# Performance work log

Hardware: AMD Instinct MI355X
Metric: run time of the kernel (lower is better)

## Reference

```python
import jax, jax.numpy as jnp
import numpy as np

N, A, AD, D, H, KTOP = 5, 900, 8, 256, 8, 300


def _bbox_min_max(anchor):
    # anchor: [N,A,8] = x,y,z,logw,logl,logh,sin_yaw,cos_yaw
    xyz = anchor[..., :3]
    w, l, h = [jnp.exp(anchor[..., i]) for i in (3, 4, 5)]
    sy, cy = anchor[..., 6], anchor[..., 7]
    yaw = jnp.arctan2(sy, cy)
    ca, sa = jnp.abs(jnp.cos(yaw)), jnp.abs(jnp.sin(yaw))
    ex = 0.5 * (l * ca + w * sa)
    ey = 0.5 * (l * sa + w * ca)
    half = jnp.stack([ex, ey, 0.5 * h], axis=-1)
    return xyz - half, xyz + half


def _forward(i2j_anchor, b_anchor, b_feature, transform_matrix, anchor_embed,
             w_roi, b_roi, bn_g, bn_b, fc1_w, fc1_b, fc2_w, fc2_b,
             anc_w, anc_b, lam_w, lam_b, wq, bq, wk, bk, wv, bv, wo, bo,
             ln_g, ln_b, K):
    n, a, ad = b_anchor.shape
    d = b_feature.shape[-1]
    heads = lam_w.shape[-1]
    dh = d // heads
    # ROI scoring + topk selection of anchors to broadcast to neighbors
    roi = jax.nn.sigmoid(b_feature @ w_roi + b_roi)[..., 0]              # [N,A]
    top_scores, top_idx = jax.lax.top_k(roi, K)                          # [N,K]
    conf = top_scores > 0.5                                              # [N,K]
    nbr = jnp.take_along_axis(b_feature, top_idx[..., None], axis=1)     # [N,K,D]
    idx4 = jnp.broadcast_to(top_idx[None, :, :, None], (n, n, K, ad))
    i2j_sel = jnp.take_along_axis(i2j_anchor, idx4, axis=2)              # [N,N,K,AD]
    # remove self (eye-mask): off-diagonal j per row i, row-major order
    offdiag = np.array([[j for j in range(n) if j != i] for i in range(n)])
    rows = np.arange(n)[:, None]
    m = K * (n - 1)
    i2j_rm = i2j_sel[rows, offdiag].reshape(n, m, ad)                    # [N,M,AD]
    tm_rm = transform_matrix[rows, offdiag]                              # [N,N-1,4,4]
    key_feat = nbr[offdiag].reshape(n, m, d)                             # [N,M,D]
    conf_rm = conf[offdiag].reshape(n, m, 1)
    nf_masked = key_feat * conf_rm
    # bbox-range masked aggregation of neighbor features into ego anchors
    mn, mx = _bbox_min_max(b_anchor)                                     # [N,A,3]
    centers = i2j_rm[..., :3]                                            # [N,M,3]
    inside = jnp.all((centers[:, None, :, :] >= mn[:, :, None, :]) &
                     (centers[:, None, :, :] <= mx[:, :, None, :]), axis=-1)  # [N,A,M]
    agg = jnp.einsum('nam,nmd->nad', inside.astype(b_feature.dtype), nf_masked)
    is_greater_than_range = ~jnp.any(inside, axis=1)                     # [N,M]
    b_feature = b_feature + agg
    # transform-matrix encoding: first 3 rows of 4x4 -> BN -> MLP
    mlp_in = tm_rm[:, :, :3, :].reshape(-1, 12)
    mu = mlp_in.mean(0)
    var = mlp_in.var(0)
    xbn = (mlp_in - mu) / jnp.sqrt(var + 1e-5) * bn_g + bn_b
    t = jax.nn.relu(xbn @ fc1_w + fc1_b) @ fc2_w + fc2_b                 # [N*(N-1),D]
    trans_enc = jnp.repeat(t.reshape(n, n - 1, 1, d), K, axis=2).reshape(n, m, d)
    key_pos = i2j_rm @ anc_w + anc_b + trans_enc                         # anchorencoder + trans
    # distance-biased attention mask
    diff = b_anchor[:, :, None, :2] - i2j_rm[:, None, :, :2]
    dist = jnp.sqrt(jnp.sum(diff * diff, axis=-1) + 1e-12)               # cdist [N,A,M]
    lm = (b_feature @ lam_w + lam_b).transpose(0, 2, 1)                  # [N,H,A]
    bias = -jnp.log1p(dist)[:, None, :, :] * lm[..., None]               # [N,H,A,M]
    # multi-head attention (query=b_feature(+anchor_embed pos), key/value=neighbors)
    q = b_feature + anchor_embed
    k = key_feat + key_pos
    v = key_feat
    qh = (q @ wq + bq).reshape(n, a, heads, dh)
    kh = (k @ wk + bk).reshape(n, m, heads, dh)
    vh = (v @ wv + bv).reshape(n, m, heads, dh)
    logits = jnp.einsum('nahd,nmhd->nham', qh, kh) / np.sqrt(dh).astype(np.float32) + bias
    attn = jax.nn.softmax(logits, axis=-1)
    out = jnp.einsum('nham,nmhd->nahd', attn, vh).reshape(n, a, d) @ wo + bo
    res = b_feature + out                                                # residual (identity=query)
    mu2 = res.mean(-1, keepdims=True)
    var2 = res.var(-1, keepdims=True)
    return (res - mu2) / jnp.sqrt(var2 + 1e-5) * ln_g + ln_b


def setup_inputs() -> dict:
    key = jax.random.key(0)
    ks = jax.random.split(key, 24)
    s = 0.05
    inp = {
        'i2j_anchor': jax.random.normal(ks[0], (N, N, A, AD), jnp.float32),
        'b_anchor': jax.random.normal(ks[1], (N, A, AD), jnp.float32),
        'b_feature': jax.random.normal(ks[2], (N, A, D), jnp.float32),
        'transform_matrix': jax.random.normal(ks[3], (N, N, 4, 4), jnp.float32),
        'anchor_embed': jax.random.normal(ks[4], (N, A, D), jnp.float32),
        'w_roi': jax.random.normal(ks[5], (D, 1), jnp.float32) * s,
        'b_roi': jnp.zeros((1,), jnp.float32),
        'bn_g': jnp.ones((12,), jnp.float32),
        'bn_b': jnp.zeros((12,), jnp.float32),
        'fc1_w': jax.random.normal(ks[6], (12, D), jnp.float32) * s,
        'fc1_b': jnp.zeros((D,), jnp.float32),
        'fc2_w': jax.random.normal(ks[7], (D, D), jnp.float32) * s,
        'fc2_b': jnp.zeros((D,), jnp.float32),
        'anc_w': jax.random.normal(ks[8], (AD, D), jnp.float32) * s,
        'anc_b': jnp.zeros((D,), jnp.float32),
        'lam_w': jax.random.normal(ks[9], (D, H), jnp.float32) * s,
        'lam_b': jnp.zeros((H,), jnp.float32),
        'wq': jax.random.normal(ks[10], (D, D), jnp.float32) * s,
        'bq': jnp.zeros((D,), jnp.float32),
        'wk': jax.random.normal(ks[11], (D, D), jnp.float32) * s,
        'bk': jnp.zeros((D,), jnp.float32),
        'wv': jax.random.normal(ks[12], (D, D), jnp.float32) * s,
        'bv': jnp.zeros((D,), jnp.float32),
        'wo': jax.random.normal(ks[13], (D, D), jnp.float32) * s,
        'bo': jnp.zeros((D,), jnp.float32),
        'ln_g': jnp.ones((D,), jnp.float32),
        'ln_b': jnp.zeros((D,), jnp.float32),
        'K': KTOP,
    }
    return inp


def reference(i2j_anchor, b_anchor, b_feature, transform_matrix, anchor_embed,
              w_roi, b_roi, bn_g, bn_b, fc1_w, fc1_b, fc2_w, fc2_b,
              anc_w, anc_b, lam_w, lam_b, wq, bq, wk, bk, wv, bv, wo, bo,
              ln_g, ln_b, K):
    return _forward(i2j_anchor, b_anchor, b_feature, transform_matrix, anchor_embed,
                    w_roi, b_roi, bn_g, bn_b, fc1_w, fc1_b, fc2_w, fc2_b,
                    anc_w, anc_b, lam_w, lam_b, wq, bq, wk, bk, wv, bv, wo, bo,
                    ln_g, ln_b, K)
```

## Files before the change

### kernel.cpp

```cpp
#include <hip/hip_runtime.h>
#include <math.h>

#define N_ 5
#define A_ 900
#define AD_ 8
#define D_ 256
#define H_ 8
#define DH_ 32
#define K_ 300
#define NM1_ 4
#define M_ 1200
#define MP_ 1216
#define KC_ 64
#define HALF_ 600
#define NCHUNK2_ 10
#define SCOREB_ 1125

typedef _Float16 f16x8 __attribute__((ext_vector_type(8)));
typedef _Float16 f16x4 __attribute__((ext_vector_type(4)));
typedef float f32x4 __attribute__((ext_vector_type(4)));

#define LOG2E_ 1.4426950408889634f

__global__ __launch_bounds__(256) void scoremlp_kernel(const float* __restrict__ bf,
                                                       const float* __restrict__ w,
                                                       const float* __restrict__ b,
                                                       const float* __restrict__ tm,
                                                       const float* __restrict__ bn_g, const float* __restrict__ bn_b,
                                                       const float* __restrict__ fc1_w, const float* __restrict__ fc1_b,
                                                       const float* __restrict__ fc2_w, const float* __restrict__ fc2_b,
                                                       float* __restrict__ scores,
                                                       float* __restrict__ t_out) {
  int bid = blockIdx.x;
  int t = threadIdx.x;
  if (bid < SCOREB_) {
    int wid = t >> 6, lane = t & 63;
    int row = bid * 4 + wid;
    if (row >= N_ * A_) return;
    const float* x = bf + (long)row * D_;
    float dot = 0.f;
#pragma unroll
    for (int e = 0; e < 4; e++) dot += x[lane + 64 * e] * w[lane + 64 * e];
#pragma unroll
    for (int o = 32; o; o >>= 1) dot += __shfl_xor(dot, o, 64);
    if (lane == 0) scores[row] = dot + b[0];
  } else {
    int r = bid - SCOREB_;
    __shared__ float x2[20][12];
    __shared__ float y2[12];
    __shared__ float hbuf[D_];
    if (t < 240) {
      int rr = t / 12, f = t % 12;
      int i = rr / NM1_, jj = rr % NM1_;
      int j = jj < i ? jj : jj + 1;
      x2[rr][f] = tm[((long)(i * N_ + j) * 4 + (f / 4)) * 4 + (f % 4)];
    }
    __syncthreads();
    if (t < 12) {
      float s = 0.f;
      for (int rr = 0; rr < 20; rr++) s += x2[rr][t];
      float m = s / 20.0f;
      float v = 0.f;
      for (int rr = 0; rr < 20; rr++) { float d = x2[rr][t] - m; v += d * d; }
      v /= 20.0f;
      y2[t] = (x2[r][t] - m) * rsqrtf(v + 1e-5f) * bn_g[t] + bn_b[t];
    }
    __syncthreads();
    float acc = fc1_b[t];
#pragma unroll
    for (int f = 0; f < 12; f++) acc += y2[f] * fc1_w[f * D_ + t];
    hbuf[t] = fmaxf(acc, 0.0f);
    __syncthreads();
    float acc2 = fc2_b[t];
    for (int k = 0; k < D_; k++) acc2 += hbuf[k] * fc2_w[k * D_ + t];
    t_out[r * D_ + t] = acc2;
  }
}

__global__ __launch_bounds__(1024) void topk_kernel(const float* __restrict__ scores,
                                                    int* __restrict__ top_idx,
                                                    float* __restrict__ conf) {
  __shared__ float sc[1024];
  __shared__ int si[1024];
  int i = blockIdx.x, t = threadIdx.x;
  sc[t] = (t < A_) ? scores[i * A_ + t] : -INFINITY;
  si[t] = t;
  __syncthreads();
  for (int k = 2; k <= 1024; k <<= 1) {
    for (int j = k >> 1; j > 0; j >>= 1) {
      int ixj = t ^ j;
      if (ixj > t) {
        bool dir = ((t & k) == 0);
        float a = sc[t], b = sc[ixj];
        bool sw = dir ? (a < b) : (a > b);
        if (sw) {
          sc[t] = b; sc[ixj] = a;
          int tmp = si[t]; si[t] = si[ixj]; si[ixj] = tmp;
        }
      }
      __syncthreads();
    }
  }
  if (t < K_) {
    top_idx[i * K_ + t] = si[t];
    conf[i * K_ + t] = sc[t] > 0.0f ? 1.0f : 0.0f;
  }
}

#define GKT_ 10
__global__ __launch_bounds__(256) void gather_kernel(const float* __restrict__ b_feature,
                                                     const float* __restrict__ i2j_anchor,
                                                     const int* __restrict__ top_idx,
                                                     const float* __restrict__ conf,
                                                     const float* __restrict__ anc_w,
                                                     const float* __restrict__ anc_b,
                                                     const float* __restrict__ t_mlp,
                                                     _Float16* __restrict__ key_feat16,
                                                     float* __restrict__ conf_rm,
                                                     float* __restrict__ i2j_rm,
                                                     _Float16* __restrict__ key_in16) {
  int blk = blockIdx.x;
  int i = blk / NM1_, jj = blk % NM1_;
  int j = jj < i ? jj : jj + 1;
  int k0 = blockIdx.y * GKT_;
  int c = threadIdx.x;
  __shared__ float aw[AD_][D_];
#pragma unroll
  for (int r = 0; r < AD_; r++) aw[r][c] = anc_w[r * D_ + c];
  float ab = anc_b[c];
  float tv = t_mlp[(i * NM1_ + jj) * D_ + c];
  __syncthreads();
  for (int k = k0; k < k0 + GKT_; k++) {
    int idx = top_idx[j * K_ + k];
    float cf = conf[j * K_ + k];
    const float* src = b_feature + ((long)(j * A_ + idx)) * D_;
    float val = src[c];
    long mrow = (long)i * M_ + jj * K_ + k;
    key_feat16[mrow * D_ + c] = (_Float16)val;
    const float* ap = i2j_anchor + ((long)((i * N_ + j) * A_ + idx)) * AD_;
    if (c < AD_) i2j_rm[mrow * AD_ + c] = ap[c];
    if (c == 0) conf_rm[mrow] = cf;
    float pos = ab + tv;
#pragma unroll
    for (int r = 0; r < AD_; r++) pos += ap[r] * aw[r][c];
    key_in16[mrow * D_ + c] = (_Float16)(val + pos);
  }
}

__global__ __launch_bounds__(256) void trans_kernel(const float* __restrict__ w0, const float* __restrict__ w1,
                                                    const float* __restrict__ w2, const float* __restrict__ w3,
                                                    const _Float16* __restrict__ kf,
                                                    _Float16* __restrict__ wT, _Float16* __restrict__ kT) {
  int bid = blockIdx.x;
  int t = threadIdx.x;
  if (bid < 64) {
    int y = bid >> 4, tile = bid & 15;
    const float* src = (y == 0) ? w0 : (y == 1) ? w1 : (y == 2) ? w2 : w3;
    _Float16* dst = wT + (size_t)y * D_ * D_;
    int kr = (tile >> 2) * 64, nc = (tile & 3) * 64;
    __shared__ float lds[64][65];
#pragma unroll
    for (int r = 0; r < 16; r++) {
      int row = r * 4 + (t >> 6), col = t & 63;
      lds[row][col] = src[(size_t)(kr + row) * D_ + nc + col];
    }
    __syncthreads();
#pragma unroll
    for (int r = 0; r < 16; r++) {
      int orow = r * 4 + (t >> 6), ocol = t & 63;
      dst[(size_t)(nc + orow) * D_ + kr + ocol] = (_Float16)lds[ocol][orow];
    }
  } else {
    int b = bid - 64;
    int i = b / 76, rem = b % 76;
    int m0 = (rem % 19) * 64, d0 = (rem / 19) * 64;
    __shared__ _Float16 lds2[64][66];
    const _Float16* src = kf + (size_t)i * M_ * D_;
    _Float16* dst = kT + (size_t)i * D_ * M_;
#pragma unroll
    for (int r = 0; r < 16; r++) {
      int row = r * 4 + (t >> 6), col = t & 63;
      int m = m0 + row;
      lds2[row][col] = (m < M_) ? src[(size_t)m * D_ + d0 + col] : (_Float16)0.0f;
    }
    __syncthreads();
#pragma unroll
    for (int r = 0; r < 16; r++) {
      int orow = r * 4 + (t >> 6), ocol = t & 63;
      int m = m0 + ocol;
      if (m < M_) dst[(size_t)(d0 + orow) * M_ + m] = lds2[ocol][orow];
    }
  }
}

__global__ __launch_bounds__(256) void insbias_kernel(const float* __restrict__ i2j_rm,
                                                      const float* __restrict__ conf_rm,
                                                      const float* __restrict__ ban,
                                                      _Float16* __restrict__ inside,
                                                      _Float16* __restrict__ Lbuf) {
  int i = blockIdx.x;
  int g = blockIdx.y;
  __shared__ float cx[M_], cy[M_], cz[M_], cf[M_];
  for (int m = threadIdx.x; m < M_; m += 256) {
    const float* cp = i2j_rm + ((long)i * M_ + m) * AD_;
    cx[m] = cp[0]; cy[m] = cp[1]; cz[m] = cp[2];
    cf[m] = conf_rm[(long)i * M_ + m];
  }
  __syncthreads();
#pragma unroll
  for (int r = 0; r < 4; r++) {
    int a = g * 4 + r;
    int row = i * A_ + a;
    const float* ap = ban + (long)row * AD_;
    float ax = ap[0], ay = ap[1], az = ap[2];
    float w = expf(ap[3]), l = expf(ap[4]), hh = expf(ap[5]);
    float yaw = atan2f(ap[6], ap[7]);
    float ca = fabsf(cosf(yaw)), sa = fabsf(sinf(yaw));
    float ex = 0.5f * (l * ca + w * sa);
    float ey = 0.5f * (l * sa + w * ca);
    float ez = 0.5f * hh;
    float mn0 = ax - ex, mn1 = ay - ey, mn2 = az - ez;
    float mx0 = ax + ex, mx1 = ay + ey, mx2 = az + ez;
    _Float16* ldst = Lbuf + (size_t)row * MP_;
    _Float16* idst = inside + (size_t)row * M_;
    for (int m = threadIdx.x; m < M_; m += 256) {
      float c0 = cx[m], c1 = cy[m], c2 = cz[m];
      bool ins = (c0 >= mn0) && (c0 <= mx0) && (c1 >= mn1) && (c1 <= mx1) && (c2 >= mn2) && (c2 <= mx2);
      idst[m] = ins ? (_Float16)cf[m] : (_Float16)0.0f;
      float dx = ax - c0, dy = ay - c1;
      ldst[m] = (_Float16)log1pf(sqrtf(dx * dx + dy * dy + 1e-12f));
    }
  }
}

#define GLD_ 74
template <typename TO, bool HAS_BIAS, bool HAS_RES, bool VTRANS = false>
__device__ __forceinline__ void gemm_tile_body(
    const _Float16* __restrict__ A, int lda, int Mr,
    const _Float16* __restrict__ B, int ldb,
    const float* __restrict__ bias, const float* __restrict__ res,
    TO* __restrict__ C, int ldc,
    int m0, int n0, int k_begin, int k_end) {
  __shared__ _Float16 As[64 * GLD_];
  __shared__ _Float16 Bs[64 * GLD_];
  int tid = threadIdx.x;
  int lane = tid & 63;
  int wid = tid >> 6;
  int wr = (wid >> 1) * 32, wc = (wid & 1) * 32;
  int lr = lane & 15, lk = (lane >> 4) * 8;
  int srow = tid >> 3;
  int scol = (tid & 7) * 8;
  f16x8 aR[2], bR[2];
  f16x8 zero8 = {};
  auto loadg = [&](int kb) {
#pragma unroll
    for (int r = 0; r < 2; r++) {
      int gm = m0 + srow + r * 32;
      int gk = kb + scol;
      aR[r] = (gm < Mr && gk < k_end) ? *(const f16x8*)&A[(size_t)gm * lda + gk] : zero8;
      int gn = n0 + srow + r * 32;
      bR[r] = (gk < k_end) ? *(const f16x8*)&B[(size_t)gn * ldb + gk] : zero8;
    }
  };
  auto store_lds = [&]() {
#pragma unroll
    for (int r = 0; r < 2; r++) {
      *(f16x8*)&As[(srow + r * 32) * GLD_ + scol] = aR[r];
      *(f16x8*)&Bs[(srow + r * 32) * GLD_ + scol] = bR[r];
    }
  };
  f32x4 acc[2][2] = {};
  int niter = (k_end - k_begin + 63) >> 6;
  loadg(k_begin);
  store_lds();
  __syncthreads();
  for (int it = 0; it < niter; ++it) {
    bool more = (it + 1 < niter);
    if (more) loadg(k_begin + (it + 1) * 64);
#pragma unroll
    for (int ks = 0; ks < 2; ks++) {
      f16x8 af[2], bf[2];
#pragma unroll
      for (int mi = 0; mi < 2; mi++) af[mi] = *(const f16x8*)&As[(wr + mi * 16 + lr) * GLD_ + ks * 32 + lk];
#pragma unroll
      for (int ni = 0; ni < 2; ni++) bf[ni] = *(const f16x8*)&Bs[(wc + ni * 16 + lr) * GLD_ + ks * 32 + lk];
#pragma unroll
      for (int mi = 0; mi < 2; mi++)
#pragma unroll
        for (int ni = 0; ni < 2; ni++)
          acc[mi][ni] = __builtin_amdgcn_mfma_f32_16x16x32_f16(af[mi], bf[ni], acc[mi][ni], 0, 0, 0);
    }
    __syncthreads();
    if (more) { store_lds(); __syncthreads(); }
  }
  if (VTRANS) {
#pragma unroll
    for (int mi = 0; mi < 2; mi++)
#pragma unroll
      for (int ni = 0; ni < 2; ni++)
#pragma unroll
        for (int rr = 0; rr < 4; rr++) {
          int ml = wr + mi * 16 + (lane >> 4) * 4 + rr;
          int dl = wc + ni * 16 + lr;
          float v = acc[mi][ni][rr];
          if (HAS_BIAS) v += bias[n0 + dl];
          As[dl * 72 + ml] = (_Float16)v;
        }
    __syncthreads();
    int dl = tid >> 2, mp = (tid & 3) * 16;
    int gd = n0 + dl;
#pragma unroll
    for (int e8 = 0; e8 < 2; e8++) {
      int gm = m0 + mp + e8 * 8;
      if (gm < Mr) {
        int ii = gm / M_, mm = gm - ii * M_;
        *(f16x8*)&((_Float16*)C)[(size_t)(ii * D_ + gd) * ldc + mm] =
            *(const f16x8*)&As[dl * 72 + mp + e8 * 8];
      }
    }
    return;
  }
#pragma unroll
  for (int mi = 0; mi < 2; mi++)
#pragma unroll
    for (int ni = 0; ni < 2; ni++)
#pragma unroll
      for (int rr = 0; rr < 4; rr++) {
        int row = m0 + wr + mi * 16 + (lane >> 4) * 4 + rr;
        int col = n0 + wc + ni * 16 + lr;
        if (row < Mr) {
          float v = acc[mi][ni][rr];
          if (HAS_BIAS) v += bias[col];
          if (HAS_RES) v += res[(size_t)row * ldc + col];
          C[(size_t)row * ldc + col] = (TO)v;
        }
      }
}

__global__ __launch_bounds__(256) void agg_kernel(const _Float16* __restrict__ inside16,
                                                  const _Float16* __restrict__ kT16,
                                                  float* __restrict__ partial) {
  int i = blockIdx.z >> 2, sk = blockIdx.z & 3;
  int kb = sk * 320;
  int ke = kb + 320 < M_ ? kb + 320 : M_;
  gemm_tile_body<float, false, false>(
      inside16 + (size_t)i * A_ * M_, M_, A_,
      kT16 + (size_t)i * D_ * M_, M_,
      nullptr, nullptr,
      partial + (size_t)(sk * N_ + i) * A_ * D_, D_,
      blockIdx.x * 64, blockIdx.y * 64, kb, ke);
}

__global__ __launch_bounds__(256) void agg_reduce(const float* __restrict__ partial,
                                                  const float* __restrict__ b_feature,
                                                  const float* __restrict__ anchor_embed,
                                                  const float* __restrict__ lam_w,
                                                  const float* __restrict__ lam_b,
                                                  float* __restrict__ bf_upd,
                                                  _Float16* __restrict__ qin16,
                                                  float* __restrict__ lm_rm) {
  int wid = threadIdx.x >> 6, lane = threadIdx.x & 63;
  int rg = blockIdx.x * 4 + wid;
  int d0 = lane * 4;
  float lw[4][8];
#pragma unroll
  for (int e = 0; e < 4; e++) {
#pragma unroll
    for (int h = 0; h < 8; h++) lw[e][h] = lam_w[(d0 + e) * 8 + h];
  }
  float4 s = *(const float4*)&partial[(size_t)rg * D_ + d0];
#pragma unroll
  for (int sk = 1; sk < 4; sk++) {
    float4 p = *(const float4*)&partial[((size_t)sk * N_ * A_ + rg) * D_ + d0];
    s.x += p.x; s.y += p.y; s.z += p.z; s.w += p.w;
  }
  float4 bf = *(const float4*)&b_feature[(size_t)rg * D_ + d0];
  s.x += bf.x; s.y += bf.y; s.z += bf.z; s.w += bf.w;
  *(float4*)&bf_upd[(size_t)rg * D_ + d0] = s;
  float4 ae = *(const float4*)&anchor_embed[(size_t)rg * D_ + d0];
  f16x4 q4;
  q4[0] = (_Float16)(s.x + ae.x); q4[1] = (_Float16)(s.y + ae.y);
  q4[2] = (_Float16)(s.z + ae.z); q4[3] = (_Float16)(s.w + ae.w);
  *(f16x4*)&qin16[(size_t)rg * D_ + d0] = q4;
  float sv[4] = {s.x, s.y, s.z, s.w};
  float acc[8] = {};
#pragma unroll
  for (int e = 0; e < 4; e++)
#pragma unroll
    for (int h = 0; h < 8; h++) acc[h] += sv[e] * lw[e][h];
#pragma unroll
  for (int h = 0; h < 8; h++) {
#pragma unroll
    for (int o = 32; o; o >>= 1) acc[h] += __shfl_xor(acc[h], o, 64);
  }
  if (lane == 0) {
#pragma unroll
    for (int h = 0; h < 8; h++) lm_rm[(size_t)rg * H_ + h] = acc[h] + lam_b[h];
  }
}

__global__ __launch_bounds__(256) void qkv_kernel(const _Float16* __restrict__ qA,
                                                  const _Float16* __restrict__ kA,
                                                  const _Float16* __restrict__ vA,
                                                  const _Float16* __restrict__ wT,
                                                  const float* __restrict__ bq,
                                                  const float* __restrict__ bk,
                                                  const float* __restrict__ bv,
                                                  _Float16* __restrict__ qC,
                                                  _Float16* __restrict__ kC,
                                                  _Float16* __restrict__ vT) {
  int bid = blockIdx.x;
  if (bid < 284) {
    int mt = bid % 71, nt = bid / 71;
    gemm_tile_body<_Float16, true, false>(qA, D_, 4500, wT, D_, bq, nullptr, qC, D_,
                                          mt * 64, nt * 64, 0, D_);
  } else if (bid < 660) {
    int t = bid - 284;
    int mt = t % 94, nt = t / 94;
    gemm_tile_body<_Float16, true, false>(kA, D_, 6000, wT + D_ * D_, D_, bk, nullptr, kC, D_,
                                          mt * 64, nt * 64, 0, D_);
  } else {
    int t = bid - 660;
    int mt = t % 94, nt = t / 94;
    gemm_tile_body<_Float16, true, false, true>(vA, D_, 6000, wT + 2 * D_ * D_, D_, bv, nullptr, vT, MP_,
                                                mt * 64, nt * 64, 0, D_);
  }
}

__global__ __launch_bounds__(256) void outp_kernel(const _Float16* __restrict__ att16,
                                                   const _Float16* __restrict__ woT,
                                                   float* __restrict__ partial2) {
  int bid = blockIdx.x;
  int sk = bid >= 284 ? 1 : 0;
  int t = bid - sk * 284;
  int mt = t % 71, nt = t / 71;
  gemm_tile_body<float, false, false>(att16, D_, 4500, woT, D_, nullptr, nullptr,
                                      partial2 + (size_t)sk * 4500 * D_, D_,
                                      mt * 64, nt * 64, sk * 128, sk * 128 + 128);
}

#define LQP_ 72
#define LKS_ 40
#define THR2_ 11.5f
__global__ __launch_bounds__(256) void attn_mfma(const _Float16* __restrict__ qh16,
                                                 const _Float16* __restrict__ kh16,
                                                 const _Float16* __restrict__ vhT,
                                                 const float* __restrict__ lm_rm,
                                                 const _Float16* __restrict__ Lbuf,
                                                 float* __restrict__ part_ms,
                                                 float* __restrict__ part_o) {
  int bid = blockIdx.x;
  int wgid = (bid & 7) * 150 + (bid >> 3);
  int ih = wgid / 30;
  int rest = wgid % 30;
  int half = rest / 15, qt = rest % 15;
  int i = ih >> 3, h = ih & 7;
  int a0 = qt * 64;
  int mbase = half * HALF_;
  int mlimit = mbase + HALF_;

  __shared__ _Float16 QP[64 * LQP_];
  __shared__ _Float16 Ks[2][64 * LKS_];
  __shared__ _Float16 Vs[2][32 * LQP_];
  __shared__ float lmvs[64];

  int tid = threadIdx.x;
  int lane = tid & 63;
  int w16 = (tid >> 6) * 16;
  int lr = lane & 15;
  int lk = (lane >> 4) * 8;
  int mq = (lane >> 4) * 4;
  int srow = tid >> 2, spiece = tid & 3;
  int vrow = tid >> 3, vpc = (tid & 7) * 8;

  {
    int aq = a0 + srow;
    int a_ld = aq < A_ ? aq : A_ - 1;
    const uint4* src = (const uint4*)(qh16 + ((long)(i * A_ + a_ld) * D_ + h * DH_));
    *(uint4*)&QP[srow * LQP_ + spiece * 8] = src[spiece];
  }
  if (tid < 64) {
    int aq = a0 + tid;
    int a_ld = aq < A_ ? aq : A_ - 1;
    lmvs[tid] = lm_rm[(long)(i * A_ + a_ld) * H_ + h];
  }

  int qrow = w16 + lr;
  const _Float16* kb = kh16 + (long)i * M_ * D_ + h * DH_;
  const _Float16* vb = vhT + (size_t)(i * D_ + h * DH_) * MP_;
  const _Float16* lq;
  {
    int aq = a0 + qrow;
    int a_ld = aq < A_ ? aq : A_ - 1;
    lq = Lbuf + (size_t)(i * A_ + a_ld) * MP_ + mq;
  }

  uint4 kvR;
  f16x8 vvR;
  f16x4 lR[4];
  auto loadr = [&](int c) {
    int m0 = mbase + c * KC_;
    int mrow = m0 + srow;
    kvR = (mrow < M_) ? ((const uint4*)(kb + (long)mrow * D_))[spiece] : make_uint4(0, 0, 0, 0);
    vvR = *(const f16x8*)&vb[(size_t)vrow * MP_ + m0 + vpc];
#pragma unroll
    for (int mb = 0; mb < 4; mb++) lR[mb] = *(const f16x4*)&lq[m0 + mb * 16];
  };

  __syncthreads();

  float lmv2 = lmvs[qrow] * LOG2E_;
  f16x8 qa = *(const f16x8*)&QP[qrow * LQP_ + lk];

  float m_run = -INFINITY, s_part = 0.0f;
  f32x4 oacc[2] = {};

  loadr(0);

  const float SC2 = 0.17677669529663687f * LOG2E_;

  auto chunk_body = [&](int c, bool masked) {
    int m0 = mbase + c * KC_;
    int cur = c & 1;
    *(uint4*)&Ks[cur][srow * LKS_ + spiece * 8] = kvR;
    *(f16x8*)&Vs[cur][vrow * LQP_ + vpc] = vvR;
    f16x4 lcur[4];
#pragma unroll
    for (int mb = 0; mb < 4; mb++) lcur[mb] = lR[mb];
    if (c + 1 < NCHUNK2_) loadr(c + 1);
    __syncthreads();

    f32x4 sacc[4];
#pragma unroll
    for (int mb = 0; mb < 4; mb++) {
      f16x8 kf = *(const f16x8*)&Ks[cur][(mb * 16 + lr) * LKS_ + lk];
      sacc[mb] = __builtin_amdgcn_mfma_f32_16x16x32_f16(kf, qa, (f32x4){0.f, 0.f, 0.f, 0.f}, 0, 0, 0);
    }

    float lg[4][4];
#pragma unroll
    for (int mb = 0; mb < 4; mb++) {
#pragma unroll
      for (int rr = 0; rr < 4; rr++) {
        float v = sacc[mb][rr] * SC2 - (float)lcur[mb][rr] * lmv2;
        if (masked) {
          int mcol = m0 + mb * 16 + mq + rr;
          v = (mcol < mlimit) ? v : -INFINITY;
        }
        lg[mb][rr] = v;
      }
    }
    float cm = -INFINITY;
#pragma unroll
    for (int mb = 0; mb < 4; mb++)
#pragma unroll
      for (int rr = 0; rr < 4; rr++) cm = fmaxf(cm, lg[mb][rr]);
    cm = fmaxf(cm, __shfl_xor(cm, 16, 64));
    cm = fmaxf(cm, __shfl_xor(cm, 32, 64));

    bool upd = !__all(cm - m_run <= THR2_);
    float corr = 1.0f;
    if (upd) {
      float nm = fmaxf(m_run, cm);
      corr = exp2f(m_run - nm);
      m_run = nm;
      lmvs[qrow] = corr;
    }
    float ps = 0.0f;
#pragma unroll
    for (int mb = 0; mb < 4; mb++) {
      f16x4 p4;
#pragma unroll
      for (int rr = 0; rr < 4; rr++) {
        float p = exp2f(lg[mb][rr] - m_run);
        ps += p;
        p4[rr] = (_Float16)p;
      }
      *(f16x4*)&QP[qrow * LQP_ + mb * 16 + mq] = p4;
    }
    if (upd) {
      float4 c4 = *(const float4*)&lmvs[w16 + mq];
      s_part = s_part * corr + ps;
      oacc[0][0] *= c4.x; oacc[0][1] *= c4.y; oacc[0][2] *= c4.z; oacc[0][3] *= c4.w;
      oacc[1][0] *= c4.x; oacc[1][1] *= c4.y; oacc[1][2] *= c4.z; oacc[1][3] *= c4.w;
    } else {
      s_part += ps;
    }

#pragma unroll
    for (int ks = 0; ks < 2; ks++) {
      f16x8 pa = *(const f16x8*)&QP[(w16 + lr) * LQP_ + ks * 32 + lk];
#pragma unroll
      for (int db = 0; db < 2; db++) {
        f16x8 vf = *(const f16x8*)&Vs[cur][(db * 16 + lr) * LQP_ + ks * 32 + lk];
        oacc[db] = __builtin_amdgcn_mfma_f32_16x16x32_f16(pa, vf, oacc[db], 0, 0, 0);
      }
    }
  };

  for (int c = 0; c < NCHUNK2_ - 1; c++) chunk_body(c, false);
  chunk_body(NCHUNK2_ - 1, true);

  float st = s_part;
  st += __shfl_xor(st, 16, 64);
  st += __shfl_xor(st, 32, 64);

  size_t base = (size_t)(half * 40 + ih) * A_;
  if (lane < 16) {
    int a = a0 + w16 + lane;
    if (a < A_) {
      part_ms[(base + a) * 2 + 0] = m_run;
      part_ms[(base + a) * 2 + 1] = st;
    }
  }
#pragma unroll
  for (int r = 0; r < 4; r++) {
    int a = a0 + w16 + mq + r;
    if (a < A_) {
      size_t rowb = base + a;
      part_o[rowb * 32 + lr] = oacc[0][r];
      part_o[rowb * 32 + 16 + lr] = oacc[1][r];
    }
  }
}

__global__ __launch_bounds__(256) void attn_merge(const float* __restrict__ part_ms,
                                                  const float* __restrict__ part_o,
                                                  _Float16* __restrict__ att16) {
  int t = threadIdx.x;
  int R = blockIdx.x * 8 + (t >> 5);
  int d = t & 31;
  int ih = R / A_, a = R % A_;
  int i = ih >> 3, h = ih & 7;
  size_t r0 = (size_t)ih * A_ + a;
  size_t r1 = (size_t)(40 + ih) * A_ + a;
  float m0 = part_ms[r0 * 2], s0 = part_ms[r0 * 2 + 1];
  float m1 = part_ms[r1 * 2], s1 = part_ms[r1 * 2 + 1];
  float M = fmaxf(m0, m1);
  float e0 = exp2f(m0 - M), e1 = exp2f(m1 - M);
  float inv = 1.0f / (s0 * e0 + s1 * e1);
  float o = part_o[r0 * 32 + d] * e0 + part_o[r1 * 32 + d] * e1;
  att16[((size_t)(i * A_ + a)) * D_ + h * DH_ + d] = (_Float16)(o * inv);
}

__global__ __launch_bounds__(256) void ln_kernel(const float* __restrict__ partial2,
                                                 const float* __restrict__ bo,
                                                 const float* __restrict__ resid,
                                                 const float* __restrict__ g,
                                                 const float* __restrict__ b,
                                                 float* __restrict__ out) {
  int row = blockIdx.x;
  int t = threadIdx.x;
  size_t idx = (size_t)row * D_ + t;
  float v = partial2[idx] + partial2[(size_t)4500 * D_ + idx] + bo[t] + resid[idx];
  float s = v, sq = v * v;
#pragma unroll
  for (int o = 32; o; o >>= 1) {
    s += __shfl_xor(s, o, 64);
    sq += __shfl_xor(sq, o, 64);
  }
  __shared__ float ss[4], ssq[4];
  int wid = t >> 6, lane = t & 63;
  if (lane == 0) { ss[wid] = s; ssq[wid] = sq; }
  __syncthreads();
  float ts = ss[0] + ss[1] + ss[2] + ss[3];
  float tq = ssq[0] + ssq[1] + ssq[2] + ssq[3];
  float mean = ts / (float)D_;
  float var = tq / (float)D_ - mean * mean;
  out[idx] = (v - mean) * rsqrtf(var + 1e-5f) * g[t] + b[t];
}

extern "C" void kernel_launch(void* const* d_in, const int* in_sizes, int n_in,
                              void* d_out, int out_size, void* d_ws, size_t ws_size,
                              hipStream_t stream) {
  const float* i2j_anchor   = (const float*)d_in[0];
  const float* b_anchor     = (const float*)d_in[1];
  const float* b_feature    = (const float*)d_in[2];
  const float* tm           = (const float*)d_in[3];
  const float* anchor_embed = (const float*)d_in[4];
  const float* w_roi  = (const float*)d_in[5];
  const float* b_roi  = (const float*)d_in[6];
  const float* bn_g   = (const float*)d_in[7];
  const float* bn_b   = (const float*)d_in[8];
  const float* fc1_w  = (const float*)d_in[9];
  const float* fc1_b  = (const float*)d_in[10];
  const float* fc2_w  = (const float*)d_in[11];
  const float* fc2_b  = (const float*)d_in[12];
  const float* anc_w  = (const float*)d_in[13];
  const float* anc_b  = (const float*)d_in[14];
  const float* lam_w  = (const float*)d_in[15];
  const float* lam_b  = (const float*)d_in[16];
  const float* wq = (const float*)d_in[17];
  const float* bq = (const float*)d_in[18];
  const float* wk = (const float*)d_in[19];
  const float* bk = (const float*)d_in[20];
  const float* wv = (const float*)d_in[21];
  const float* bv = (const float*)d_in[22];
  const float* wo = (const float*)d_in[23];
  const float* bo = (const float*)d_in[24];
  const float* ln_g = (const float*)d_in[25];
  const float* ln_b = (const float*)d_in[26];

  float* ws = (float*)d_ws;
  size_t off = 0;
  auto alloc = [&](size_t n) { float* p = ws + off; off += (n + 3) & ~(size_t)3; return p; };

  float* scores     = alloc(N_ * A_);
  int*   top_idx    = (int*)alloc(N_ * K_);
  float* conf       = alloc(N_ * K_);
  float* t_mlp      = alloc(20 * D_);
  float* conf_rm    = alloc((size_t)N_ * M_);
  float* i2j_rm     = alloc((size_t)N_ * M_ * AD_);
  _Float16* key_feat16 = (_Float16*)alloc((size_t)N_ * M_ * D_ / 2);
  _Float16* key_in16   = (_Float16*)alloc((size_t)N_ * M_ * D_ / 2);
  _Float16* kT16       = (_Float16*)alloc((size_t)N_ * D_ * M_ / 2);
  _Float16* inside16   = (_Float16*)alloc((size_t)N_ * A_ * M_ / 2);
  _Float16* wT16       = (_Float16*)alloc((size_t)4 * D_ * D_ / 2);
  _Float16* Lbuf16     = (_Float16*)alloc((size_t)N_ * A_ * MP_ / 2 + 16);
  float* partial    = alloc((size_t)4 * N_ * A_ * D_);
  float* bf_upd     = alloc((size_t)N_ * A_ * D_);
  _Float16* qin16   = (_Float16*)alloc((size_t)N_ * A_ * D_ / 2);
  _Float16* qh16    = (_Float16*)alloc((size_t)N_ * A_ * D_ / 2);
  _Float16* kh16    = (_Float16*)alloc((size_t)N_ * M_ * D_ / 2);
  _Float16* vhT16   = (_Float16*)alloc((size_t)N_ * D_ * MP_ / 2 + 16);
  float* lm_rm      = alloc((size_t)N_ * A_ * H_);
  _Float16* att16   = (_Float16*)alloc((size_t)N_ * A_ * D_ / 2);
  float* partial2   = alloc((size_t)2 * N_ * A_ * D_);
  float* part_ms    = alloc((size_t)2 * 40 * A_ * 2);
  float* part_o     = alloc((size_t)2 * 40 * A_ * 32);

  scoremlp_kernel<<<SCOREB_ + 20, 256, 0, stream>>>(b_feature, w_roi, b_roi, tm,
                                                    bn_g, bn_b, fc1_w, fc1_b, fc2_w, fc2_b,
                                                    scores, t_mlp);
  topk_kernel<<<N_, 1024, 0, stream>>>(scores, top_idx, conf);
  gather_kernel<<<dim3(N_ * NM1_, K_ / GKT_), 256, 0, stream>>>(b_feature, i2j_anchor, top_idx, conf,
                                                                anc_w, anc_b, t_mlp,
                                                                key_feat16, conf_rm, i2j_rm, key_in16);
  trans_kernel<<<64 + 380, 256, 0, stream>>>(wq, wk, wv, wo, key_feat16, wT16, kT16);
  insbias_kernel<<<dim3(N_, A_ / 4), 256, 0, stream>>>(i2j_rm, conf_rm, b_anchor, inside16, Lbuf16);
  agg_kernel<<<dim3(15, 4, N_ * 4), 256, 0, stream>>>(inside16, kT16, partial);
  agg_reduce<<<(N_ * A_) / 4, 256, 0, stream>>>(partial, b_feature, anchor_embed, lam_w, lam_b,
                                                bf_upd, qin16, lm_rm);
  qkv_kernel<<<284 + 376 + 376, 256, 0, stream>>>(qin16, key_in16, key_feat16, wT16,
                                                  bq, bk, bv, qh16, kh16, vhT16);
  attn_mfma<<<1200, 256, 0, stream>>>(qh16, kh16, vhT16, lm_rm, Lbuf16, part_ms, part_o);
  attn_merge<<<(40 * A_) / 8, 256, 0, stream>>>(part_ms, part_o, att16);
  outp_kernel<<<568, 256, 0, stream>>>(att16, wT16 + 3 * D_ * D_, partial2);
  ln_kernel<<<N_ * A_, 256, 0, stream>>>(partial2, bo, bf_upd, ln_g, ln_b, (float*)d_out);
}
```

Measured before the change: 173.6 us.

## Merge weight transpose into score kernel and key transpose into insbias kernel

Moves the fp16 weight transposes into the score/MLP kernel as extra blocks, and merges the key-feature transpose into the insbias kernel, removing one launch. The shared GEMM tile body is templated on K-tile depth and the QKV and output projections use a 128-deep K tile, which halves K iterations and barriers at the cost of more shared memory. The attention kernel now does the cross-lane max shuffle only when a running-max update is needed. These changes aim to cut launch overhead and synchronization, but may lower occupancy from the larger shared allocations.

Result: faster. 170.2 us (-2.0%).

```diff
diff --git a/kernel.cpp b/kernel.cpp
--- a/kernel.cpp
+++ b/kernel.cpp
@@ -29,8 +29,12 @@
                                                        const float* __restrict__ bn_g, const float* __restrict__ bn_b,
                                                        const float* __restrict__ fc1_w, const float* __restrict__ fc1_b,
                                                        const float* __restrict__ fc2_w, const float* __restrict__ fc2_b,
+                                                       const float* __restrict__ w0, const float* __restrict__ w1,
+                                                       const float* __restrict__ w2, const float* __restrict__ w3,
                                                        float* __restrict__ scores,
-                                                       float* __restrict__ t_out) {
+                                                       float* __restrict__ t_out,
+                                                       _Float16* __restrict__ wT) {
+  __shared__ __align__(16) char smem[64 * 65 * 4];
   int bid = blockIdx.x;
   int t = threadIdx.x;
   if (bid < SCOREB_) {
@@ -44,26 +48,26 @@
 #pragma unroll
     for (int o = 32; o; o >>= 1) dot += __shfl_xor(dot, o, 64);
     if (lane == 0) scores[row] = dot + b[0];
-  } else {
+  } else if (bid < SCOREB_ + 20) {
     int r = bid - SCOREB_;
-    __shared__ float x2[20][12];
-    __shared__ float y2[12];
-    __shared__ float hbuf[D_];
+    float* x2 = (float*)smem;
+    float* y2 = x2 + 240;
+    float* hbuf = y2 + 12;
     if (t < 240) {
       int rr = t / 12, f = t % 12;
       int i = rr / NM1_, jj = rr % NM1_;
       int j = jj < i ? jj : jj + 1;
-      x2[rr][f] = tm[((long)(i * N_ + j) * 4 + (f / 4)) * 4 + (f % 4)];
+      x2[rr * 12 + f] = tm[((long)(i * N_ + j) * 4 + (f / 4)) * 4 + (f % 4)];
     }
     __syncthreads();
     if (t < 12) {
       float s = 0.f;
-      for (int rr = 0; rr < 20; rr++) s += x2[rr][t];
+      for (int rr = 0; rr < 20; rr++) s += x2[rr * 12 + t];
       float m = s / 20.0f;
       float v = 0.f;
-      for (int rr = 0; rr < 20; rr++) { float d = x2[rr][t] - m; v += d * d; }
+      for (int rr = 0; rr < 20; rr++) { float d = x2[rr * 12 + t] - m; v += d * d; }
       v /= 20.0f;
-      y2[t] = (x2[r][t] - m) * rsqrtf(v + 1e-5f) * bn_g[t] + bn_b[t];
+      y2[t] = (x2[r * 12 + t] - m) * rsqrtf(v + 1e-5f) * bn_g[t] + bn_b[t];
     }
     __syncthreads();
     float acc = fc1_b[t];
@@ -74,6 +78,24 @@
     float acc2 = fc2_b[t];
     for (int k = 0; k < D_; k++) acc2 += hbuf[k] * fc2_w[k * D_ + t];
     t_out[r * D_ + t] = acc2;
+  } else {
+    int wb = bid - (SCOREB_ + 20);
+    int y = wb >> 4, tile = wb & 15;
+    const float* src = (y == 0) ? w0 : (y == 1) ? w1 : (y == 2) ? w2 : w3;
+    _Float16* dst = wT + (size_t)y * D_ * D_;
+    int kr = (tile >> 2) * 64, nc = (tile & 3) * 64;
+    float* lds = (float*)smem;
+#pragma unroll
+    for (int r = 0; r < 16; r++) {
+      int row = r * 4 + (t >> 6), col = t & 63;
+      lds[row * 65 + col] = src[(size_t)(kr + row) * D_ + nc + col];
+    }
+    __syncthreads();
+#pragma unroll
+    for (int r = 0; r < 16; r++) {
+      int orow = r * 4 + (t >> 6), ocol = t & 63;
+      dst[(size_t)(nc + orow) * D_ + kr + ocol] = (_Float16)lds[ocol * 65 + orow];
+    }
   }
 }
 
@@ -147,143 +169,130 @@
   }
 }
 
-__global__ __launch_bounds__(256) void trans_kernel(const float* __restrict__ w0, const float* __restrict__ w1,
-                                                    const float* __restrict__ w2, const float* __restrict__ w3,
-                                                    const _Float16* __restrict__ kf,
-                                                    _Float16* __restrict__ wT, _Float16* __restrict__ kT) {
+__global__ __launch_bounds__(256) void insbias_kernel(const float* __restrict__ i2j_rm,
+                                                      const float* __restrict__ conf_rm,
+                                                      const float* __restrict__ ban,
+                                                      const _Float16* __restrict__ kf,
+                                                      _Float16* __restrict__ inside,
+                                                      _Float16* __restrict__ Lbuf,
+                                                      _Float16* __restrict__ kT) {
+  __shared__ __align__(16) char smem[4 * M_ * 4];
   int bid = blockIdx.x;
-  int t = threadIdx.x;
-  if (bid < 64) {
-    int y = bid >> 4, tile = bid & 15;
-    const float* src = (y == 0) ? w0 : (y == 1) ? w1 : (y == 2) ? w2 : w3;
-    _Float16* dst = wT + (size_t)y * D_ * D_;
-    int kr = (tile >> 2) * 64, nc = (tile & 3) * 64;
-    __shared__ float lds[64][65];
-#pragma unroll
-    for (int r = 0; r < 16; r++) {
-      int row = r * 4 + (t >> 6), col = t & 63;
-      lds[row][col] = src[(size_t)(kr + row) * D_ + nc + col];
-    }
-    __syncthreads();
-#pragma unroll
-    for (int r = 0; r < 16; r++) {
-      int orow = r * 4 + (t >> 6), ocol = t & 63;
-      dst[(size_t)(nc + orow) * D_ + kr + ocol] = (_Float16)lds[ocol][orow];
+  if (bid < SCOREB_) {
+    int i = bid / 225;
+    int g = bid % 225;
+    float* cx = (float*)smem;
+    float* cy = cx + M_;
+    float* cz = cy + M_;
+    float* cf = cz + M_;
+    for (int m = threadIdx.x; m < M_; m += 256) {
+      const float* cp = i2j_rm + ((long)i * M_ + m) * AD_;
+      cx[m] = cp[0]; cy[m] = cp[1]; cz[m] = cp[2];
+      cf[m] = conf_rm[(long)i * M_ + m];
+    }
+    __syncthreads();
+#pragma unroll
+    for (int r = 0; r < 4; r++) {
+      int a = g * 4 + r;
+      int row = i * A_ + a;
+      const float* ap = ban + (long)row * AD_;
+      float ax = ap[0], ay = ap[1], az = ap[2];
+      float w = expf(ap[3]), l = expf(ap[4]), hh = expf(ap[5]);
+      float yaw = atan2f(ap[6], ap[7]);
+      float ca = fabsf(cosf(yaw)), sa = fabsf(sinf(yaw));
+      float ex = 0.5f * (l * ca + w * sa);
+      float ey = 0.5f * (l * sa + w * ca);
+      float ez = 0.5f * hh;
+      float mn0 = ax - ex, mn1 = ay - ey, mn2 = az - ez;
+      float mx0 = ax + ex, mx1 = ay + ey, mx2 = az + ez;
+      _Float16* ldst = Lbuf + (size_t)row * MP_;
+      _Float16* idst = inside + (size_t)row * M_;
+      for (int m = threadIdx.x; m < M_; m += 256) {
+        float c0 = cx[m], c1 = cy[m], c2 = cz[m];
+        bool ins = (c0 >= mn0) && (c0 <= mx0) && (c1 >= mn1) && (c1 <= mx1) && (c2 >= mn2) && (c2 <= mx2);
+        idst[m] = ins ? (_Float16)cf[m] : (_Float16)0.0f;
+        float dx = ax - c0, dy = ay - c1;
+        ldst[m] = (_Float16)log1pf(sqrtf(dx * dx + dy * dy + 1e-12f));
+      }
     }
   } else {
-    int b = bid - 64;
+    int b = bid - SCOREB_;
     int i = b / 76, rem = b % 76;
     int m0 = (rem % 19) * 64, d0 = (rem / 19) * 64;
-    __shared__ _Float16 lds2[64][66];
+    int t = threadIdx.x;
+    _Float16* lds2 = (_Float16*)smem;
     const _Float16* src = kf + (size_t)i * M_ * D_;
     _Float16* dst = kT + (size_t)i * D_ * M_;
 #pragma unroll
     for (int r = 0; r < 16; r++) {
       int row = r * 4 + (t >> 6), col = t & 63;
       int m = m0 + row;
-      lds2[row][col] = (m < M_) ? src[(size_t)m * D_ + d0 + col] : (_Float16)0.0f;
+      lds2[row * 66 + col] = (m < M_) ? src[(size_t)m * D_ + d0 + col] : (_Float16)0.0f;
     }
     __syncthreads();
 #pragma unroll
     for (int r = 0; r < 16; r++) {
       int orow = r * 4 + (t >> 6), ocol = t & 63;
       int m = m0 + ocol;
-      if (m < M_) dst[(size_t)(d0 + orow) * M_ + m] = lds2[ocol][orow];
-    }
-  }
-}
-
-__global__ __launch_bounds__(256) void insbias_kernel(const float* __restrict__ i2j_rm,
-                                                      const float* __restrict__ conf_rm,
-                                                      const float* __restrict__ ban,
-                                                      _Float16* __restrict__ inside,
-                                                      _Float16* __restrict__ Lbuf) {
-  int i = blockIdx.x;
-  int g = blockIdx.y;
-  __shared__ float cx[M_], cy[M_], cz[M_], cf[M_];
-  for (int m = threadIdx.x; m < M_; m += 256) {
-    const float* cp = i2j_rm + ((long)i * M_ + m) * AD_;
-    cx[m] = cp[0]; cy[m] = cp[1]; cz[m] = cp[2];
-    cf[m] = conf_rm[(long)i * M_ + m];
-  }
-  __syncthreads();
-#pragma unroll
-  for (int r = 0; r < 4; r++) {
-    int a = g * 4 + r;
-    int row = i * A_ + a;
-    const float* ap = ban + (long)row * AD_;
-    float ax = ap[0], ay = ap[1], az = ap[2];
-    float w = expf(ap[3]), l = expf(ap[4]), hh = expf(ap[5]);
-    float yaw = atan2f(ap[6], ap[7]);
-    float ca = fabsf(cosf(yaw)), sa = fabsf(sinf(yaw));
-    float ex = 0.5f * (l * ca + w * sa);
-    float ey = 0.5f * (l * sa + w * ca);
-    float ez = 0.5f * hh;
-    float mn0 = ax - ex, mn1 = ay - ey, mn2 = az - ez;
-    float mx0 = ax + ex, mx1 = ay + ey, mx2 = az + ez;
-    _Float16* ldst = Lbuf + (size_t)row * MP_;
-    _Float16* idst = inside + (size_t)row * M_;
-    for (int m = threadIdx.x; m < M_; m += 256) {
-      float c0 = cx[m], c1 = cy[m], c2 = cz[m];
-      bool ins = (c0 >= mn0) && (c0 <= mx0) && (c1 >= mn1) && (c1 <= mx1) && (c2 >= mn2) && (c2 <= mx2);
-      idst[m] = ins ? (_Float16)cf[m] : (_Float16)0.0f;
-      float dx = ax - c0, dy = ay - c1;
-      ldst[m] = (_Float16)log1pf(sqrtf(dx * dx + dy * dy + 1e-12f));
-    }
-  }
-}
-
-#define GLD_ 74
-template <typename TO, bool HAS_BIAS, bool HAS_RES, bool VTRANS = false>
+      if (m < M_) dst[(size_t)(d0 + orow) * M_ + m] = lds2[ocol * 66 + orow];
+    }
+  }
+}
+
+template <int BK, typename TO, bool HAS_BIAS, bool HAS_RES, bool VTRANS = false>
 __device__ __forceinline__ void gemm_tile_body(
     const _Float16* __restrict__ A, int lda, int Mr,
     const _Float16* __restrict__ B, int ldb,
     const float* __restrict__ bias, const float* __restrict__ res,
     TO* __restrict__ C, int ldc,
     int m0, int n0, int k_begin, int k_end) {
-  __shared__ _Float16 As[64 * GLD_];
-  __shared__ _Float16 Bs[64 * GLD_];
+  constexpr int GLD = BK + 8;
+  constexpr int CPR = BK / 8;
+  constexpr int RPP = 256 / CPR;
+  constexpr int NL = 64 / RPP;
+  __shared__ _Float16 As[64 * GLD];
+  __shared__ _Float16 Bs[64 * GLD];
   int tid = threadIdx.x;
   int lane = tid & 63;
   int wid = tid >> 6;
   int wr = (wid >> 1) * 32, wc = (wid & 1) * 32;
   int lr = lane & 15, lk = (lane >> 4) * 8;
-  int srow = tid >> 3;
-  int scol = (tid & 7) * 8;
-  f16x8 aR[2], bR[2];
+  int srow = tid / CPR;
+  int scol = (tid % CPR) * 8;
+  f16x8 aR[NL], bR[NL];
   f16x8 zero8 = {};
   auto loadg = [&](int kb) {
 #pragma unroll
-    for (int r = 0; r < 2; r++) {
-      int gm = m0 + srow + r * 32;
+    for (int r = 0; r < NL; r++) {
+      int gm = m0 + srow + r * RPP;
       int gk = kb + scol;
       aR[r] = (gm < Mr && gk < k_end) ? *(const f16x8*)&A[(size_t)gm * lda + gk] : zero8;
-      int gn = n0 + srow + r * 32;
+      int gn = n0 + srow + r * RPP;
       bR[r] = (gk < k_end) ? *(const f16x8*)&B[(size_t)gn * ldb + gk] : zero8;
     }
   };
   auto store_lds = [&]() {
 #pragma unroll
-    for (int r = 0; r < 2; r++) {
-      *(f16x8*)&As[(srow + r * 32) * GLD_ + scol] = aR[r];
-      *(f16x8*)&Bs[(srow + r * 32) * GLD_ + scol] = bR[r];
+    for (int r = 0; r < NL; r++) {
+      *(f16x8*)&As[(srow + r * RPP) * GLD + scol] = aR[r];
+      *(f16x8*)&Bs[(srow + r * RPP) * GLD + scol] = bR[r];
     }
   };
   f32x4 acc[2][2] = {};
-  int niter = (k_end - k_begin + 63) >> 6;
+  int niter = (k_end - k_begin + BK - 1) / BK;
   loadg(k_begin);
   store_lds();
   __syncthreads();
   for (int it = 0; it < niter; ++it) {
     bool more = (it + 1 < niter);
-    if (more) loadg(k_begin + (it + 1) * 64);
-#pragma unroll
-    for (int ks = 0; ks < 2; ks++) {
+    if (more) loadg(k_begin + (it + 1) * BK);
+#pragma unroll
+    for (int ks = 0; ks < BK / 32; ks++) {
       f16x8 af[2], bf[2];
 #pragma unroll
-      for (int mi = 0; mi < 2; mi++) af[mi] = *(const f16x8*)&As[(wr + mi * 16 + lr) * GLD_ + ks * 32 + lk];
-#pragma unroll
-      for (int ni = 0; ni < 2; ni++) bf[ni] = *(const f16x8*)&Bs[(wc + ni * 16 + lr) * GLD_ + ks * 32 + lk];
+      for (int mi = 0; mi < 2; mi++) af[mi] = *(const f16x8*)&As[(wr + mi * 16 + lr) * GLD + ks * 32 + lk];
+#pragma unroll
+      for (int ni = 0; ni < 2; ni++) bf[ni] = *(const f16x8*)&Bs[(wc + ni * 16 + lr) * GLD + ks * 32 + lk];
 #pragma unroll
       for (int mi = 0; mi < 2; mi++)
 #pragma unroll
@@ -343,7 +352,7 @@
   int i = blockIdx.z >> 2, sk = blockIdx.z & 3;
   int kb = sk * 320;
   int ke = kb + 320 < M_ ? kb + 320 : M_;
-  gemm_tile_body<float, false, false>(
+  gemm_tile_body<64, float, false, false>(
       inside16 + (size_t)i * A_ * M_, M_, A_,
       kT16 + (size_t)i * D_ * M_, M_,
       nullptr, nullptr,
@@ -412,18 +421,18 @@
   int bid = blockIdx.x;
   if (bid < 284) {
     int mt = bid % 71, nt = bid / 71;
-    gemm_tile_body<_Float16, true, false>(qA, D_, 4500, wT, D_, bq, nullptr, qC, D_,
-                                          mt * 64, nt * 64, 0, D_);
+    gemm_tile_body<128, _Float16, true, false>(qA, D_, 4500, wT, D_, bq, nullptr, qC, D_,
+                                               mt * 64, nt * 64, 0, D_);
   } else if (bid < 660) {
     int t = bid - 284;
     int mt = t % 94, nt = t / 94;
-    gemm_tile_body<_Float16, true, false>(kA, D_, 6000, wT + D_ * D_, D_, bk, nullptr, kC, D_,
-                                          mt * 64, nt * 64, 0, D_);
+    gemm_tile_body<128, _Float16, true, false>(kA, D_, 6000, wT + D_ * D_, D_, bk, nullptr, kC, D_,
+                                               mt * 64, nt * 64, 0, D_);
   } else {
     int t = bid - 660;
     int mt = t % 94, nt = t / 94;
-    gemm_tile_body<_Float16, true, false, true>(vA, D_, 6000, wT + 2 * D_ * D_, D_, bv, nullptr, vT, MP_,
-                                                mt * 64, nt * 64, 0, D_);
+    gemm_tile_body<128, _Float16, true, false, true>(vA, D_, 6000, wT + 2 * D_ * D_, D_, bv, nullptr, vT, MP_,
+                                                     mt * 64, nt * 64, 0, D_);
   }
 }
 
@@ -434,9 +443,9 @@
   int sk = bid >= 284 ? 1 : 0;
   int t = bid - sk * 284;
   int mt = t % 71, nt = t / 71;
-  gemm_tile_body<float, false, false>(att16, D_, 4500, woT, D_, nullptr, nullptr,
-                                      partial2 + (size_t)sk * 4500 * D_, D_,
-                                      mt * 64, nt * 64, sk * 128, sk * 128 + 128);
+  gemm_tile_body<128, float, false, false>(att16, D_, 4500, woT, D_, nullptr, nullptr,
+                                           partial2 + (size_t)sk * 4500 * D_, D_,
+                                           mt * 64, nt * 64, sk * 128, sk * 128 + 128);
 }
 
 #define LQP_ 72
@@ -550,17 +559,17 @@
         lg[mb][rr] = v;
       }
     }
-    float cm = -INFINITY;
+    float cmL = -INFINITY;
 #pragma unroll
     for (int mb = 0; mb < 4; mb++)
 #pragma unroll
-      for (int rr = 0; rr < 4; rr++) cm = fmaxf(cm, lg[mb][rr]);
-    cm = fmaxf(cm, __shfl_xor(cm, 16, 64));
-    cm = fmaxf(cm, __shfl_xor(cm, 32, 64));
-
-    bool upd = !__all(cm - m_run <= THR2_);
+      for (int rr = 0; rr < 4; rr++) cmL = fmaxf(cmL, lg[mb][rr]);
+
+    bool upd = !__all(cmL - m_run <= THR2_);
     float corr = 1.0f;
     if (upd) {
+      float cm = fmaxf(cmL, __shfl_xor(cmL, 16, 64));
+      cm = fmaxf(cm, __shfl_xor(cm, 32, 64));
       float nm = fmaxf(m_run, cm);
       corr = exp2f(m_run - nm);
       m_run = nm;
@@ -729,15 +738,16 @@
   float* part_ms    = alloc((size_t)2 * 40 * A_ * 2);
   float* part_o     = alloc((size_t)2 * 40 * A_ * 32);
 
-  scoremlp_kernel<<<SCOREB_ + 20, 256, 0, stream>>>(b_feature, w_roi, b_roi, tm,
-                                                    bn_g, bn_b, fc1_w, fc1_b, fc2_w, fc2_b,
-                                                    scores, t_mlp);
+  scoremlp_kernel<<<SCOREB_ + 20 + 64, 256, 0, stream>>>(b_feature, w_roi, b_roi, tm,
+                                                         bn_g, bn_b, fc1_w, fc1_b, fc2_w, fc2_b,
+                                                         wq, wk, wv, wo,
+                                                         scores, t_mlp, wT16);
   topk_kernel<<<N_, 1024, 0, stream>>>(scores, top_idx, conf);
   gather_kernel<<<dim3(N_ * NM1_, K_ / GKT_), 256, 0, stream>>>(b_feature, i2j_anchor, top_idx, conf,
                                                                 anc_w, anc_b, t_mlp,
                                                                 key_feat16, conf_rm, i2j_rm, key_in16);
-  trans_kernel<<<64 + 380, 256, 0, stream>>>(wq, wk, wv, wo, key_feat16, wT16, kT16);
-  insbias_kernel<<<dim3(N_, A_ / 4), 256, 0, stream>>>(i2j_rm, conf_rm, b_anchor, inside16, Lbuf16);
+  insbias_kernel<<<SCOREB_ + 380, 256, 0, stream>>>(i2j_rm, conf_rm, b_anchor, key_feat16,
+                                                    inside16, Lbuf16, kT16);
   agg_kernel<<<dim3(15, 4, N_ * 4), 256, 0, stream>>>(inside16, kT16, partial);
   agg_reduce<<<(N_ * A_) / 4, 256, 0, stream>>>(partial, b_feature, anchor_embed, lam_w, lam_b,
                                                 bf_upd, qin16, lm_rm);
```
